# Kernel optimization log

Measured on AMD Instinct MI355X. Metric: run time of the kernel, lower is better.

Reference implementation:

```python
import jax, jax.numpy as jnp
import numpy as np

B, S, N, BS, D, H, V = 1, 2048, 128, 16, 512, 8, 32000
MASK_TOKEN_ID = 3


def setup_inputs() -> dict:
    key = jax.random.key(0)
    ks = jax.random.split(key, 10)
    anchors = jnp.sort(jax.random.randint(ks[0], (B, N), 0, S - BS), axis=1)
    return {
        "input_ids": jax.random.randint(ks[1], (B, S), 0, V),
        "hidden_states": jax.random.normal(ks[2], (B, S, D), dtype=jnp.float32),
        "loss_mask": jnp.ones((B, S), dtype=jnp.float32),
        "anchor_positions": anchors,
        "block_keep_mask": jnp.ones((B, N), dtype=bool),
        "embed_table": jax.random.normal(ks[3], (V, D), dtype=jnp.float32) * 0.02,
        "Wq": jax.random.normal(ks[4], (D, D), dtype=jnp.float32) * 0.02,
        "Wk": jax.random.normal(ks[5], (D, D), dtype=jnp.float32) * 0.02,
        "Wv": jax.random.normal(ks[6], (D, D), dtype=jnp.float32) * 0.02,
        "Wo": jax.random.normal(ks[7], (D, D), dtype=jnp.float32) * 0.02,
        "W_lm": jax.random.normal(ks[8], (D, V), dtype=jnp.float32) * 0.02,
    }


def dflash_sdpa_mask(anchor_positions, block_keep_mask):
    # KV layout: [context S | block_0 .. block_{N-1}], Q layout: [block_0 .. block_{N-1}]
    Q = N * BS
    KV = S + N * BS
    q_idx = jnp.arange(Q)              # [Q]
    kv_idx = jnp.arange(KV)            # [KV]
    q_blk = q_idx // BS                # [Q]
    anchor_q = anchor_positions[:, q_blk]          # [B,Q] anchor of each query's block
    keep_q = block_keep_mask[:, q_blk]             # [B,Q]
    is_ctx = kv_idx < S                             # [KV]
    mask_context = is_ctx[None, None, :] & (kv_idx[None, None, :] < anchor_q[:, :, None])  # [B,Q,KV]
    kv_blk = (kv_idx - S) // BS
    mask_draft = (kv_idx >= S)[None, :] & (q_blk[:, None] == kv_blk[None, :])              # [Q,KV]
    final = (mask_context | mask_draft[None]) & keep_q[:, :, None]                          # [B,Q,KV]
    return final


def reference(input_ids, hidden_states, loss_mask, anchor_positions, block_keep_mask,
              embed_table, Wq, Wk, Wv, Wo, W_lm):
    dh = D // H
    Q = N * BS

    # --- noise embedding: MASK token everywhere, anchor token at each block start ---
    safe_anchor = jnp.clip(anchor_positions, 0, S - 1)                     # [B,N]
    anchor_tokens = jnp.take_along_axis(input_ids, safe_anchor, axis=1)    # [B,N]
    start_tokens = jnp.where(block_keep_mask, anchor_tokens, MASK_TOKEN_ID)
    noise_ids = jnp.full((B, Q), MASK_TOKEN_ID, dtype=input_ids.dtype)
    noise_ids = noise_ids.at[:, jnp.arange(N) * BS].set(start_tokens)
    noise_embedding = embed_table[noise_ids]                               # [B,Q,D]

    # --- draft attention: Q = draft tokens, KV = [context hiddens | draft tokens] ---
    kv_in = jnp.concatenate([hidden_states, noise_embedding], axis=1)      # [B,S+Q,D]
    q = (noise_embedding @ Wq).reshape(B, Q, H, dh)
    k = (kv_in @ Wk).reshape(B, S + Q, H, dh)
    v = (kv_in @ Wv).reshape(B, S + Q, H, dh)
    scores = jnp.einsum("bqhd,bkhd->bhqk", q, k) / jnp.sqrt(jnp.float32(dh))
    mask = dflash_sdpa_mask(anchor_positions, block_keep_mask)[:, None]    # [B,1,Q,KV]
    attn = jax.nn.softmax(jnp.where(mask, scores, -1e9), axis=-1)
    out = jnp.einsum("bhqk,bkhd->bqhd", attn, v).reshape(B, Q, D) @ Wo     # [B,Q,D]
    logits = out @ W_lm                                                    # [B,Q,V]

    # --- block-wise CE loss ---
    offs = jnp.arange(BS)
    label_idx = anchor_positions[:, :, None] + offs[None, None, :]         # [B,N,BS]
    valid_label = label_idx < S
    safe_idx = jnp.clip(label_idx, 0, S - 1)
    ids_b = jnp.broadcast_to(input_ids[:, None, :], (B, N, S))
    target_ids = jnp.take_along_axis(ids_b, safe_idx, axis=2)              # [B,N,BS]
    lm_b = jnp.broadcast_to(loss_mask[:, None, :], (B, N, S))
    lm_g = jnp.take_along_axis(lm_b, safe_idx, axis=2)
    weight = (block_keep_mask[:, :, None].astype(jnp.float32)
              * valid_label.astype(jnp.float32)
              * (offs > 0)[None, None, :].astype(jnp.float32)
              * lm_g)                                                      # [B,N,BS]

    flat_logits = logits.reshape(-1, V)
    flat_targets = target_ids.reshape(-1)
    flat_w = weight.reshape(-1)
    logp = jax.nn.log_softmax(flat_logits, axis=-1)
    loss_per = -jnp.take_along_axis(logp, flat_targets[:, None], axis=1)[:, 0]
    loss = jnp.sum(loss_per * flat_w) / (jnp.sum(flat_w) + 1e-6)

    pred = jnp.argmax(flat_logits, axis=-1)
    correct = (pred == flat_targets) & (flat_w > 0.5)
    accuracy = jnp.sum(correct).astype(jnp.float32) / (jnp.sum(flat_w) + 1e-6)
    return loss, accuracy
```

## Files before the change

### kernel.cpp

```cpp
#include <hip/hip_runtime.h>

typedef unsigned short u16;
typedef __attribute__((ext_vector_type(4))) float f32x4;
typedef __attribute__((ext_vector_type(8))) short short8;
typedef __attribute__((ext_vector_type(4))) unsigned int uv4;
typedef __attribute__((ext_vector_type(4))) float fv4;
typedef __attribute__((ext_vector_type(4))) unsigned short usv4;

#define S_LEN 2048
#define NBLK 128
#define DMODEL 512
#define VOCAB 32000
#define QLEN 2048
#define KVLEN 4096
#define NSPLIT 250

#define GAS(p) ((const __attribute__((address_space(1))) void*)(const void*)(p))
#define LAS(p) ((__attribute__((address_space(3))) void*)(void*)(p))

__device__ __forceinline__ float bf2f(u16 u){
  union { unsigned int i; float f; } x; x.i = ((unsigned int)u) << 16; return x.f;
}
__device__ __forceinline__ u16 f2bf(float f){
  union { float f; unsigned int i; } x; x.f = f;
  unsigned int r = x.i + 0x7fffu + ((x.i >> 16) & 1u);
  return (u16)(r >> 16);
}

__global__ __launch_bounds__(256) void transpose4(const float* __restrict__ i0, const float* __restrict__ i1,
                                                  const float* __restrict__ i2, const float* __restrict__ i3,
                                                  u16* __restrict__ o0, u16* __restrict__ o1,
                                                  u16* __restrict__ o2, u16* __restrict__ o3){
  const float* in; u16* out;
  switch (blockIdx.z){
    case 0: in = i0; out = o0; break;
    case 1: in = i1; out = o1; break;
    case 2: in = i2; out = o2; break;
    default: in = i3; out = o3; break;
  }
  __shared__ float tile[32][33];
  int t = threadIdx.x, tx = t & 31, ty = t >> 5;
  int nb = blockIdx.x * 32, kb = blockIdx.y * 32;
  #pragma unroll
  for (int i = 0; i < 4; i++){
    int r = ty + i * 8;
    tile[r][tx] = in[(size_t)(kb + r) * 512 + nb + tx];
  }
  __syncthreads();
  #pragma unroll
  for (int i = 0; i < 4; i++){
    int r = ty + i * 8;
    out[(size_t)(nb + r) * 512 + kb + tx] = f2bf(tile[tx][r]);
  }
}

__global__ __launch_bounds__(256) void transpose_cast(const float* __restrict__ in,
                                                      u16* __restrict__ out,
                                                      int K, int N){
  __shared__ float tile[32][33];
  int t = threadIdx.x, tx = t & 31, ty = t >> 5;
  int nb = blockIdx.x * 32, kb = blockIdx.y * 32;
  #pragma unroll
  for (int i = 0; i < 4; i++){
    int r = ty + i * 8;
    tile[r][tx] = in[(size_t)(kb + r) * N + nb + tx];
  }
  __syncthreads();
  #pragma unroll
  for (int i = 0; i < 4; i++){
    int r = ty + i * 8;
    out[(size_t)(nb + r) * K + kb + tx] = f2bf(tile[tx][r]);
  }
}

__global__ __launch_bounds__(128) void build_kv(const float* __restrict__ hidden,
                                                const float* __restrict__ embed,
                                                const int* __restrict__ input_ids,
                                                const int* __restrict__ anchors,
                                                const unsigned char* __restrict__ keep,
                                                u16* __restrict__ kvb){
  int row = blockIdx.x;
  int t = threadIdx.x;
  const float* src;
  if (row < S_LEN){
    src = hidden + (size_t)row * DMODEL;
  } else {
    int q = row - S_LEN;
    int id = 3;
    if ((q & 15) == 0){
      int n = q >> 4;
      if (keep[n]){
        int a = anchors[n]; a = min(max(a, 0), S_LEN - 1);
        id = input_ids[a];
      }
    }
    src = embed + (size_t)id * DMODEL;
  }
  int c = t * 4;
  fv4 v = *(const fv4*)&src[c];
  usv4 o; o[0] = f2bf(v[0]); o[1] = f2bf(v[1]); o[2] = f2bf(v[2]); o[3] = f2bf(v[3]);
  *(usv4*)&kvb[(size_t)row * DMODEL + c] = o;
}

template<int TRANS, int MF>
__global__ __launch_bounds__(256) void gemmTile(const u16* __restrict__ A,
                                                const u16* __restrict__ BT,
                                                u16* __restrict__ C,
                                                int M, int N, int K, int ldc){
  __shared__ __align__(16) u16 As[2][64 * MF * 64];
  __shared__ __align__(16) u16 Bs[2][64 * 64];
  int t = threadIdx.x, w = t >> 6, lane = t & 63;
  int g = lane >> 4, li = lane & 15;
  int rowbase = blockIdx.x * (64 * MF), colbase = blockIdx.y * 64;
  int r0 = t >> 3, cg0 = t & 7;
  int swz = (cg0 ^ (r0 & 7)) << 3;

  auto stageA = [&](u16* dst, int kb){
    #pragma unroll
    for (int i = 0; i < 2 * MF; i++)
      __builtin_amdgcn_global_load_lds(GAS(&A[(size_t)(rowbase + r0 + i * 32) * K + kb + swz]),
                                       LAS(dst + i * 2048 + w * 512), 16, 0, 0);
  };
  auto stageB = [&](u16* dst, int kb){
    #pragma unroll
    for (int i = 0; i < 2; i++)
      __builtin_amdgcn_global_load_lds(GAS(&BT[(size_t)(colbase + r0 + i * 32) * K + kb + swz]),
                                       LAS(dst + i * 2048 + w * 512), 16, 0, 0);
  };

  f32x4 acc[MF][4];
  #pragma unroll
  for (int i = 0; i < MF; i++)
    #pragma unroll
    for (int j = 0; j < 4; j++)
      acc[i][j] = (f32x4){0.f, 0.f, 0.f, 0.f};

  stageA(As[0], 0); stageB(Bs[0], 0);

  int nkt = K >> 6;
  for (int kt = 0; kt < nkt; kt++){
    u16* curA = As[kt & 1]; u16* curB = Bs[kt & 1];
    if (kt + 1 < nkt){
      stageA(As[(kt + 1) & 1], (kt + 1) * 64); stageB(Bs[(kt + 1) & 1], (kt + 1) * 64);
      if constexpr (MF == 2) asm volatile("s_waitcnt vmcnt(6)" ::: "memory");
      else                   asm volatile("s_waitcnt vmcnt(4)" ::: "memory");
    } else {
      asm volatile("s_waitcnt vmcnt(0)" ::: "memory");
    }
    __builtin_amdgcn_s_barrier();
    #pragma unroll
    for (int ks = 0; ks < 2; ks++){
      short8 af[MF], bf[4];
      #pragma unroll
      for (int mf = 0; mf < MF; mf++){
        int row = w * 16 * MF + mf * 16 + li;
        af[mf] = *(const short8*)&curA[row * 64 + (((ks * 4 + g) ^ (li & 7)) << 3)];
      }
      #pragma unroll
      for (int nf = 0; nf < 4; nf++){
        int row = nf * 16 + li;
        bf[nf] = *(const short8*)&curB[row * 64 + (((ks * 4 + g) ^ (li & 7)) << 3)];
      }
      #pragma unroll
      for (int mf = 0; mf < MF; mf++)
        #pragma unroll
        for (int nf = 0; nf < 4; nf++)
          acc[mf][nf] = __builtin_amdgcn_mfma_f32_16x16x32_bf16(af[mf], bf[nf], acc[mf][nf], 0, 0, 0);
    }
    __builtin_amdgcn_s_barrier();
  }

  #pragma unroll
  for (int mf = 0; mf < MF; mf++)
    #pragma unroll
    for (int nf = 0; nf < 4; nf++)
      #pragma unroll
      for (int r = 0; r < 4; r++){
        int row = rowbase + w * 16 * MF + mf * 16 + g * 4 + r;
        int col = colbase + nf * 16 + li;
        u16 vv = f2bf(acc[mf][nf][r]);
        if (TRANS) C[(size_t)col * ldc + row] = vv;
        else       C[(size_t)row * ldc + col] = vv;
      }
}

__global__ __launch_bounds__(256) void attn_mfma(const u16* __restrict__ qb,
                                                 const u16* __restrict__ kb,
                                                 const u16* __restrict__ vT,
                                                 const int* __restrict__ anchors,
                                                 const unsigned char* __restrict__ keep,
                                                 u16* __restrict__ attnb){
  int n = blockIdx.x, h = blockIdx.y;
  int t = threadIdx.x, w = t >> 6, lane = t & 63;
  int g = lane >> 4, li = lane & 15;

  __shared__ __align__(16) u16 q_s[16][72];
  __shared__ __align__(16) u16 p_s[4][16][72];
  __shared__ float o_s[4][16][64];
  __shared__ float ml_s[4][2][16];

  {
    int r = t >> 4, c4 = (t & 15) * 4;
    *(usv4*)&q_s[r][c4] = *(const usv4*)&qb[(size_t)(n * 16 + r) * DMODEL + h * 64 + c4];
  }
  __syncthreads();

  int anchor = anchors[n];
  bool kp = keep[n] != 0;
  const u16* kh  = kb + h * 64;
  const u16* vTh = vT + (size_t)(h * 64) * KVLEN;

  if (!kp){
    if (w == 0){
      float acc = 0.f;
      const u16* row = vTh + (size_t)lane * KVLEN;
      for (int k2 = 0; k2 < KVLEN; k2 += 8){
        short8 vv = *(const short8*)&row[k2];
        #pragma unroll
        for (int j = 0; j < 8; j++) acc += bf2f((u16)vv[j]);
      }
      acc *= (1.f / 4096.f);
      u16 ov = f2bf(acc);
      for (int r = 0; r < 16; r++)
        attnb[(size_t)(n * 16 + r) * DMODEL + h * 64 + lane] = ov;
    }
    return;
  }

  short8 qa[2];
  #pragma unroll
  for (int ks = 0; ks < 2; ks++)
    qa[ks] = *(const short8*)&q_s[li][ks * 32 + g * 8];

  int nctx = (anchor + 63) >> 6;
  int ntot = nctx + 1;

  f32x4 o_acc[4];
  float m[4], l[4];
  #pragma unroll
  for (int i = 0; i < 4; i++){ o_acc[i] = (f32x4){0.f,0.f,0.f,0.f}; m[i] = -3e38f; l[i] = 0.f; }

  for (int c = w; c < ntot; c += 4){
    bool draft = (c == nctx);
    int kbase = draft ? (S_LEN + n * 16) : c * 64;
    int nk    = draft ? 16 : min(64, anchor - c * 64);

    f32x4 s[4];
    #pragma unroll
    for (int nf = 0; nf < 4; nf++) s[nf] = (f32x4){0.f,0.f,0.f,0.f};
    #pragma unroll
    for (int ks = 0; ks < 2; ks++){
      #pragma unroll
      for (int nf = 0; nf < 4; nf++){
        int krow = min(kbase + nf * 16 + li, KVLEN - 1);
        short8 bfrag = *(const short8*)&kh[(size_t)krow * DMODEL + ks * 32 + g * 8];
        s[nf] = __builtin_amdgcn_mfma_f32_16x16x32_bf16(qa[ks], bfrag, s[nf], 0, 0, 0);
      }
    }

    #pragma unroll
    for (int r = 0; r < 4; r++){
      float mx = -3e38f;
      #pragma unroll
      for (int nf = 0; nf < 4; nf++){
        float sv = s[nf][r] * 0.125f;
        if (nf * 16 + li >= nk) sv = -3e38f;
        s[nf][r] = sv;
        mx = fmaxf(mx, sv);
      }
      #pragma unroll
      for (int mm = 1; mm < 16; mm <<= 1) mx = fmaxf(mx, __shfl_xor(mx, mm));
      float mn = fmaxf(m[r], mx);
      float sc = __expf(m[r] - mn);
      float ps = 0.f;
      #pragma unroll
      for (int nf = 0; nf < 4; nf++){
        float p = __expf(s[nf][r] - mn);
        ps += p;
        p_s[w][g * 4 + r][nf * 16 + li] = f2bf(p);
      }
      #pragma unroll
      for (int mm = 1; mm < 16; mm <<= 1) ps += __shfl_xor(ps, mm);
      l[r] = l[r] * sc + ps;
      m[r] = mn;
      #pragma unroll
      for (int nfd = 0; nfd < 4; nfd++) o_acc[nfd][r] *= sc;
    }

    #pragma unroll
    for (int ks = 0; ks < 2; ks++){
      short8 pa = *(const short8*)&p_s[w][li][ks * 32 + g * 8];
      int kcol = min(kbase + ks * 32 + g * 8, KVLEN - 8);
      #pragma unroll
      for (int nfd = 0; nfd < 4; nfd++){
        short8 vfrag = *(const short8*)&vTh[(size_t)(nfd * 16 + li) * KVLEN + kcol];
        o_acc[nfd] = __builtin_amdgcn_mfma_f32_16x16x32_bf16(pa, vfrag, o_acc[nfd], 0, 0, 0);
      }
    }
  }

  #pragma unroll
  for (int r = 0; r < 4; r++){
    if (li == 0){ ml_s[w][0][g * 4 + r] = m[r]; ml_s[w][1][g * 4 + r] = l[r]; }
    #pragma unroll
    for (int nfd = 0; nfd < 4; nfd++)
      o_s[w][g * 4 + r][nfd * 16 + li] = o_acc[nfd][r];
  }
  __syncthreads();

  {
    int row = t >> 4, c0 = (t & 15) * 4;
    float M = -3e38f;
    #pragma unroll
    for (int ww = 0; ww < 4; ww++) M = fmaxf(M, ml_s[ww][0][row]);
    float L = 0.f, ew[4];
    #pragma unroll
    for (int ww = 0; ww < 4; ww++){
      ew[ww] = __expf(ml_s[ww][0][row] - M);
      L += ml_s[ww][1][row] * ew[ww];
    }
    float inv = 1.f / L;
    #pragma unroll
    for (int j = 0; j < 4; j++){
      float ov = 0.f;
      #pragma unroll
      for (int ww = 0; ww < 4; ww++) ov += o_s[ww][row][c0 + j] * ew[ww];
      attnb[(size_t)(n * 16 + row) * DMODEL + h * 64 + c0 + j] = f2bf(ov * inv);
    }
  }
}

__global__ __launch_bounds__(256) void lm_fused(const u16* __restrict__ obp,
                                                const u16* __restrict__ WT,
                                                const int* __restrict__ input_ids,
                                                const int* __restrict__ anchors,
                                                float* __restrict__ pl,
                                                float* __restrict__ pt, float* __restrict__ pbv,
                                                int* __restrict__ pbi){
  __shared__ __align__(16) u16 Wb[2][128 * 32];
  __shared__ __align__(16) u16 Ob[2][128 * 32];
  __shared__ int tcol_s[128];

  int L = blockIdx.x;
  int T = (L & 7) * 500 + (L >> 3);
  int qbase = (T & 15) * 128;
  int vb = T >> 4;
  int vocabbase = vb * 128;
  int t = threadIdx.x, w = t >> 6, lane = t & 63;
  int g = lane >> 4, li = lane & 15;
  int wv = w & 1, wq = w >> 1;

  if (t < 128){
    int r = qbase + t; int n = r >> 4, off = r & 15;
    int lab = anchors[n] + off;
    int safe = min(max(lab, 0), S_LEN - 1);
    tcol_s[t] = input_ids[safe];
  }

  int sr = t >> 2;
  int scg = (t & 3) ^ ((sr >> 1) & 3);
  auto stage = [&](u16* wdst, u16* odst, int kb){
    #pragma unroll
    for (int i = 0; i < 2; i++){
      __builtin_amdgcn_global_load_lds(GAS(&WT [(size_t)(vocabbase + i * 64 + sr) * DMODEL + kb + (scg << 3)]),
                                       LAS(wdst + i * 2048 + w * 512), 16, 0, 0);
      __builtin_amdgcn_global_load_lds(GAS(&obp[(size_t)(qbase     + i * 64 + sr) * DMODEL + kb + (scg << 3)]),
                                       LAS(odst + i * 2048 + w * 512), 16, 0, 0);
    }
  };

  f32x4 acc[4][4];
  #pragma unroll
  for (int i = 0; i < 4; i++)
    #pragma unroll
    for (int j = 0; j < 4; j++)
      acc[i][j] = (f32x4){0.f, 0.f, 0.f, 0.f};

  stage(Wb[0], Ob[0], 0);

  int cgr = (g ^ ((li >> 1) & 3)) << 3;
  for (int kt = 0; kt < 16; kt++){
    const u16* curW = Wb[kt & 1]; const u16* curO = Ob[kt & 1];
    if (kt < 15){
      stage(Wb[(kt + 1) & 1], Ob[(kt + 1) & 1], (kt + 1) * 32);
      asm volatile("s_waitcnt vmcnt(4)" ::: "memory");
    } else {
      asm volatile("s_waitcnt vmcnt(0)" ::: "memory");
    }
    __builtin_amdgcn_s_barrier();
    __builtin_amdgcn_s_setprio(1);
    short8 wfr[4], obf[4];
    #pragma unroll
    for (int vf = 0; vf < 4; vf++)
      wfr[vf] = *(const short8*)&curW[(wv * 64 + vf * 16 + li) * 32 + cgr];
    #pragma unroll
    for (int qf = 0; qf < 4; qf++)
      obf[qf] = *(const short8*)&curO[(wq * 64 + qf * 16 + li) * 32 + cgr];
    #pragma unroll
    for (int vf = 0; vf < 4; vf++)
      #pragma unroll
      for (int qf = 0; qf < 4; qf++)
        acc[vf][qf] = __builtin_amdgcn_mfma_f32_16x16x32_bf16(wfr[vf], obf[qf], acc[vf][qf], 0, 0, 0);
    __builtin_amdgcn_s_setprio(0);
    __builtin_amdgcn_s_barrier();
  }
  __syncthreads();

  u16* sb = &Wb[0][0];
  float* cse = (float*)(sb);
  float* ctv = (float*)(sb + 512);
  float* cbv = (float*)(sb + 1024);
  int*   cbi = (int*)  (sb + 1536);

  #pragma unroll
  for (int qf = 0; qf < 4; qf++){
    int qloc = wq * 64 + qf * 16 + li;
    int tc = tcol_s[qloc] - (vocabbase + wv * 64);
    float se = 0.f, tv = -3e38f, bv = -3e38f; int bi = 0x7fffffff;
    #pragma unroll
    for (int vf = 0; vf < 4; vf++){
      #pragma unroll
      for (int r = 0; r < 4; r++){
        float v = acc[vf][qf][r];
        int pos = vf * 16 + g * 4 + r;
        se += __expf(v);
        if (pos == tc) tv = v;
        if (v > bv){ bv = v; bi = pos; }
      }
    }
    #pragma unroll
    for (int off = 16; off <= 32; off <<= 1){
      se += __shfl_xor(se, off);
      tv = fmaxf(tv, __shfl_xor(tv, off));
      float ob_ = __shfl_xor(bv, off); int oi = __shfl_xor(bi, off);
      if (ob_ > bv || (ob_ == bv && oi < bi)){ bv = ob_; bi = oi; }
    }
    if (g == 0){
      cse[wv * 128 + qloc] = se; ctv[wv * 128 + qloc] = tv;
      cbv[wv * 128 + qloc] = bv; cbi[wv * 128 + qloc] = wv * 64 + bi;
    }
  }
  __syncthreads();

  if (t < 128){
    float SE = 0.f, TV = -3e38f, BV = -3e38f; int BI = 0x7fffffff;
    #pragma unroll
    for (int vv = 0; vv < 2; vv++){
      SE += cse[vv * 128 + t];
      TV = fmaxf(TV, ctv[vv * 128 + t]);
      float v = cbv[vv * 128 + t];
      if (v > BV){ BV = v; BI = cbi[vv * 128 + t]; }
    }
    size_t idx = (size_t)vb * QLEN + qbase + t;
    pl[idx] = SE; pt[idx] = TV; pbv[idx] = BV; pbi[idx] = vocabbase + BI;
  }
}

__global__ __launch_bounds__(256) void loss_rows(const float* __restrict__ pl,
                                                 const float* __restrict__ pt, const float* __restrict__ pbv,
                                                 const int* __restrict__ pbi,
                                                 const int* __restrict__ input_ids,
                                                 const int* __restrict__ anchors,
                                                 const unsigned char* __restrict__ keep,
                                                 const float* __restrict__ loss_mask,
                                                 float* __restrict__ rowacc){
  int t = threadIdx.x, w = t >> 6, lane = t & 63;
  int row = blockIdx.x * 4 + w;
  float L = 0.f, TV = -3e38f, BV = -3e38f; int BI = 0x7fffffff;
  for (int s = lane; s < NSPLIT; s += 64){
    size_t idx = (size_t)s * QLEN + row;
    L += pl[idx];
    TV = fmaxf(TV, pt[idx]);
    float bv_ = pbv[idx]; int bi_ = pbi[idx];
    if (bv_ > BV || (bv_ == BV && bi_ < BI)){ BV = bv_; BI = bi_; }
  }
  #pragma unroll
  for (int mm = 1; mm < 64; mm <<= 1){
    L += __shfl_xor(L, mm);
    TV = fmaxf(TV, __shfl_xor(TV, mm));
    float ob = __shfl_xor(BV, mm); int oi = __shfl_xor(BI, mm);
    if (ob > BV || (ob == BV && oi < BI)){ BV = ob; BI = oi; }
  }
  if (lane == 0){
    int n = row >> 4, off = row & 15;
    int lab = anchors[n] + off;
    int valid = (lab < S_LEN) ? 1 : 0;
    int safe = min(max(lab, 0), S_LEN - 1);
    int tgt = input_ids[safe];
    float wgt = (keep[n] ? 1.f : 0.f) * (valid ? 1.f : 0.f) * ((off > 0) ? 1.f : 0.f) * loss_mask[safe];
    float logp = TV - __logf(L);
    rowacc[row * 3 + 0] = -logp * wgt;
    rowacc[row * 3 + 1] = wgt;
    rowacc[row * 3 + 2] = ((BI == tgt) && (wgt > 0.5f)) ? 1.f : 0.f;
  }
}

__global__ __launch_bounds__(256) void final_sum(const float* __restrict__ rowacc, float* __restrict__ out){
  int t = threadIdx.x;
  float a = 0.f, b = 0.f, c = 0.f;
  for (int r = t; r < QLEN; r += 256){
    a += rowacc[r * 3 + 0]; b += rowacc[r * 3 + 1]; c += rowacc[r * 3 + 2];
  }
  __shared__ float sa[256], sb[256], sc_[256];
  sa[t] = a; sb[t] = b; sc_[t] = c;
  __syncthreads();
  for (int s = 128; s >= 1; s >>= 1){
    if (t < s){ sa[t] += sa[t + s]; sb[t] += sb[t + s]; sc_[t] += sc_[t + s]; }
    __syncthreads();
  }
  if (t == 0){
    out[0] = sa[0] / (sb[0] + 1e-6f);
    out[1] = sc_[0] / (sb[0] + 1e-6f);
  }
}

extern "C" void kernel_launch(void* const* d_in, const int* in_sizes, int n_in,
                              void* d_out, int out_size, void* d_ws, size_t ws_size,
                              hipStream_t stream) {
  const int*   input_ids = (const int*)  d_in[0];
  const float* hidden    = (const float*)d_in[1];
  const float* loss_mask = (const float*)d_in[2];
  const int*   anchors   = (const int*)  d_in[3];
  const unsigned char* keep = (const unsigned char*)d_in[4];
  const float* embed     = (const float*)d_in[5];
  const float* Wq        = (const float*)d_in[6];
  const float* Wk        = (const float*)d_in[7];
  const float* Wv        = (const float*)d_in[8];
  const float* Wo        = (const float*)d_in[9];
  const float* Wlm       = (const float*)d_in[10];

  char* ws = (char*)d_ws;
  size_t off = 0;
  auto take = [&](size_t bytes) -> char* {
    char* p = ws + off;
    off += (bytes + 255) & ~(size_t)255;
    return p;
  };
  u16* WqT  = (u16*)take((size_t)512 * 512 * 2);
  u16* WkT  = (u16*)take((size_t)512 * 512 * 2);
  u16* WvT  = (u16*)take((size_t)512 * 512 * 2);
  u16* WoT  = (u16*)take((size_t)512 * 512 * 2);
  u16* WlmT = (u16*)take((size_t)VOCAB * 512 * 2);
  u16* kvb  = (u16*)take((size_t)KVLEN * 512 * 2);
  u16* qb2  = (u16*)take((size_t)QLEN * 512 * 2);
  u16* kb   = (u16*)take((size_t)KVLEN * 512 * 2);
  u16* vTb  = (u16*)take((size_t)512 * KVLEN * 2);
  u16* attnb= (u16*)take((size_t)QLEN * 512 * 2);
  u16* ob   = (u16*)take((size_t)QLEN * 512 * 2);
  float* pl = (float*)take((size_t)QLEN * NSPLIT * 4);
  float* pt = (float*)take((size_t)QLEN * NSPLIT * 4);
  float* pbv= (float*)take((size_t)QLEN * NSPLIT * 4);
  int*   pbi= (int*)  take((size_t)QLEN * NSPLIT * 4);
  float* rowacc = (float*)take((size_t)QLEN * 3 * 4);

  transpose4<<<dim3(16, 16, 4), 256, 0, stream>>>(Wq, Wk, Wv, Wo, WqT, WkT, WvT, WoT);
  transpose_cast<<<dim3(1000, 16), 256, 0, stream>>>(Wlm, WlmT, 512, VOCAB);

  build_kv<<<KVLEN, 128, 0, stream>>>(hidden, embed, input_ids, anchors, keep, kvb);

  gemmTile<0, 2><<<dim3(32, 8), 256, 0, stream>>>(kvb, WkT, kb,  KVLEN, 512, 512, 512);
  gemmTile<1, 2><<<dim3(32, 8), 256, 0, stream>>>(kvb, WvT, vTb, KVLEN, 512, 512, KVLEN);
  gemmTile<0, 1><<<dim3(32, 8), 256, 0, stream>>>(kvb + (size_t)S_LEN * 512, WqT, qb2, QLEN, 512, 512, 512);

  attn_mfma<<<dim3(NBLK, 8), 256, 0, stream>>>(qb2, kb, vTb, anchors, keep, attnb);

  gemmTile<0, 1><<<dim3(32, 8), 256, 0, stream>>>(attnb, WoT, ob, QLEN, 512, 512, 512);

  lm_fused<<<4000, 256, 0, stream>>>(ob, WlmT, input_ids, anchors, pl, pt, pbv, pbi);

  loss_rows<<<512, 256, 0, stream>>>(pl, pt, pbv, pbi, input_ids, anchors, keep, loss_mask, rowacc);

  final_sum<<<1, 256, 0, stream>>>(rowacc, (float*)d_out);
}
```

Measured before the change: 235.4 us.

## Pre-swizzle LM weights into MFMA fragment layout and merge QKV GEMMs

The LM-head weight is transposed into a layout where each lane's MFMA B-fragment is one contiguous 16-byte chunk. lm_fused can then load weight fragments straight from global memory into registers, skipping LDS staging for W and halving its LDS footprint. The three Q/K/V projection GEMMs are merged into a single 640-block launch, and the Q and O projections move from 64-row to 128-row tiles. The risks are exposed global-load latency in the LM loop, now covered only by the vmcnt waits, and fewer blocks for the O projection.

```diff
diff --git a/kernel.cpp b/kernel.cpp
--- a/kernel.cpp
+++ b/kernel.cpp
@@ -54,23 +54,26 @@
   }
 }
 
-__global__ __launch_bounds__(256) void transpose_cast(const float* __restrict__ in,
-                                                      u16* __restrict__ out,
-                                                      int K, int N){
+__global__ __launch_bounds__(256) void transpose_wlm_frag(const float* __restrict__ in,
+                                                          u16* __restrict__ Wf){
   __shared__ float tile[32][33];
   int t = threadIdx.x, tx = t & 31, ty = t >> 5;
-  int nb = blockIdx.x * 32, kb = blockIdx.y * 32;
+  int vb32 = blockIdx.x, kt = blockIdx.y;
   #pragma unroll
   for (int i = 0; i < 4; i++){
     int r = ty + i * 8;
-    tile[r][tx] = in[(size_t)(kb + r) * N + nb + tx];
+    tile[r][tx] = in[(size_t)(kt * 32 + r) * VOCAB + vb32 * 32 + tx];
   }
   __syncthreads();
-  #pragma unroll
-  for (int i = 0; i < 4; i++){
-    int r = ty + i * 8;
-    out[(size_t)(nb + r) * K + kb + tx] = f2bf(tile[tx][r]);
-  }
+  int v_local = t >> 3, gg = t & 7;
+  int g = gg >> 1, j0 = (gg & 1) * 4;
+  int v = vb32 * 32 + v_local;
+  int v16 = v >> 4, li = v & 15;
+  usv4 o;
+  #pragma unroll
+  for (int jj = 0; jj < 4; jj++)
+    o[jj] = f2bf(tile[g * 8 + j0 + jj][v_local]);
+  *(usv4*)&Wf[(size_t)(((v16 * 16 + kt) * 64) + g * 16 + li) * 8 + j0] = o;
 }
 
 __global__ __launch_bounds__(128) void build_kv(const float* __restrict__ hidden,
@@ -102,58 +105,151 @@
   *(usv4*)&kvb[(size_t)row * DMODEL + c] = o;
 }
 
-template<int TRANS, int MF>
-__global__ __launch_bounds__(256) void gemmTile(const u16* __restrict__ A,
-                                                const u16* __restrict__ BT,
-                                                u16* __restrict__ C,
-                                                int M, int N, int K, int ldc){
-  __shared__ __align__(16) u16 As[2][64 * MF * 64];
+__global__ __launch_bounds__(256) void qkv_gemm(const u16* __restrict__ kvb,
+                                                const u16* __restrict__ WkT,
+                                                const u16* __restrict__ WvT,
+                                                const u16* __restrict__ WqT,
+                                                u16* __restrict__ kb,
+                                                u16* __restrict__ vTb,
+                                                u16* __restrict__ qb2){
+  __shared__ __align__(16) u16 As[2][128 * 64];
+  __shared__ __align__(16) u16 Bs[2][64 * 64];
+  int id = blockIdx.x;
+  const u16* A = kvb; const u16* BT; u16* C; int ldc; int trans = 0;
+  int rowbase, colbase;
+  if (id < 256){
+    BT = WkT; C = kb; ldc = 512;
+    rowbase = (id & 31) * 128; colbase = (id >> 5) * 64;
+  } else if (id < 512){
+    int j = id - 256;
+    BT = WvT; C = vTb; ldc = KVLEN; trans = 1;
+    rowbase = (j & 31) * 128; colbase = (j >> 5) * 64;
+  } else {
+    int j = id - 512;
+    A = kvb + (size_t)S_LEN * DMODEL;
+    BT = WqT; C = qb2; ldc = 512;
+    rowbase = (j & 15) * 128; colbase = (j >> 4) * 64;
+  }
+  int t = threadIdx.x, w = t >> 6, lane = t & 63;
+  int g = lane >> 4, li = lane & 15;
+  int r0 = t >> 3, cg0 = t & 7;
+  int swz = (cg0 ^ (r0 & 7)) << 3;
+
+  auto stageA = [&](u16* dst, int kb_){
+    #pragma unroll
+    for (int i = 0; i < 4; i++)
+      __builtin_amdgcn_global_load_lds(GAS(&A[(size_t)(rowbase + r0 + i * 32) * DMODEL + kb_ + swz]),
+                                       LAS(dst + i * 2048 + w * 512), 16, 0, 0);
+  };
+  auto stageB = [&](u16* dst, int kb_){
+    #pragma unroll
+    for (int i = 0; i < 2; i++)
+      __builtin_amdgcn_global_load_lds(GAS(&BT[(size_t)(colbase + r0 + i * 32) * DMODEL + kb_ + swz]),
+                                       LAS(dst + i * 2048 + w * 512), 16, 0, 0);
+  };
+
+  f32x4 acc[2][4];
+  #pragma unroll
+  for (int i = 0; i < 2; i++)
+    #pragma unroll
+    for (int j = 0; j < 4; j++)
+      acc[i][j] = (f32x4){0.f, 0.f, 0.f, 0.f};
+
+  stageA(As[0], 0); stageB(Bs[0], 0);
+
+  for (int kt = 0; kt < 8; kt++){
+    u16* curA = As[kt & 1]; u16* curB = Bs[kt & 1];
+    if (kt < 7){
+      stageA(As[(kt + 1) & 1], (kt + 1) * 64); stageB(Bs[(kt + 1) & 1], (kt + 1) * 64);
+      asm volatile("s_waitcnt vmcnt(6)" ::: "memory");
+    } else {
+      asm volatile("s_waitcnt vmcnt(0)" ::: "memory");
+    }
+    __builtin_amdgcn_s_barrier();
+    #pragma unroll
+    for (int ks = 0; ks < 2; ks++){
+      short8 af[2], bf[4];
+      #pragma unroll
+      for (int mf = 0; mf < 2; mf++){
+        int row = w * 32 + mf * 16 + li;
+        af[mf] = *(const short8*)&curA[row * 64 + (((ks * 4 + g) ^ (li & 7)) << 3)];
+      }
+      #pragma unroll
+      for (int nf = 0; nf < 4; nf++){
+        int row = nf * 16 + li;
+        bf[nf] = *(const short8*)&curB[row * 64 + (((ks * 4 + g) ^ (li & 7)) << 3)];
+      }
+      #pragma unroll
+      for (int mf = 0; mf < 2; mf++)
+        #pragma unroll
+        for (int nf = 0; nf < 4; nf++)
+          acc[mf][nf] = __builtin_amdgcn_mfma_f32_16x16x32_bf16(af[mf], bf[nf], acc[mf][nf], 0, 0, 0);
+    }
+    __builtin_amdgcn_s_barrier();
+  }
+
+  #pragma unroll
+  for (int mf = 0; mf < 2; mf++)
+    #pragma unroll
+    for (int nf = 0; nf < 4; nf++)
+      #pragma unroll
+      for (int r = 0; r < 4; r++){
+        int row = rowbase + w * 32 + mf * 16 + g * 4 + r;
+        int col = colbase + nf * 16 + li;
+        u16 vv = f2bf(acc[mf][nf][r]);
+        if (trans) C[(size_t)col * ldc + row] = vv;
+        else       C[(size_t)row * ldc + col] = vv;
+      }
+}
+
+__global__ __launch_bounds__(256) void gemmO(const u16* __restrict__ A,
+                                             const u16* __restrict__ BT,
+                                             u16* __restrict__ C){
+  __shared__ __align__(16) u16 As[2][128 * 64];
   __shared__ __align__(16) u16 Bs[2][64 * 64];
   int t = threadIdx.x, w = t >> 6, lane = t & 63;
   int g = lane >> 4, li = lane & 15;
-  int rowbase = blockIdx.x * (64 * MF), colbase = blockIdx.y * 64;
+  int rowbase = blockIdx.x * 128, colbase = blockIdx.y * 64;
   int r0 = t >> 3, cg0 = t & 7;
   int swz = (cg0 ^ (r0 & 7)) << 3;
 
-  auto stageA = [&](u16* dst, int kb){
-    #pragma unroll
-    for (int i = 0; i < 2 * MF; i++)
-      __builtin_amdgcn_global_load_lds(GAS(&A[(size_t)(rowbase + r0 + i * 32) * K + kb + swz]),
+  auto stageA = [&](u16* dst, int kb_){
+    #pragma unroll
+    for (int i = 0; i < 4; i++)
+      __builtin_amdgcn_global_load_lds(GAS(&A[(size_t)(rowbase + r0 + i * 32) * DMODEL + kb_ + swz]),
                                        LAS(dst + i * 2048 + w * 512), 16, 0, 0);
   };
-  auto stageB = [&](u16* dst, int kb){
+  auto stageB = [&](u16* dst, int kb_){
     #pragma unroll
     for (int i = 0; i < 2; i++)
-      __builtin_amdgcn_global_load_lds(GAS(&BT[(size_t)(colbase + r0 + i * 32) * K + kb + swz]),
+      __builtin_amdgcn_global_load_lds(GAS(&BT[(size_t)(colbase + r0 + i * 32) * DMODEL + kb_ + swz]),
                                        LAS(dst + i * 2048 + w * 512), 16, 0, 0);
   };
 
-  f32x4 acc[MF][4];
-  #pragma unroll
-  for (int i = 0; i < MF; i++)
+  f32x4 acc[2][4];
+  #pragma unroll
+  for (int i = 0; i < 2; i++)
     #pragma unroll
     for (int j = 0; j < 4; j++)
       acc[i][j] = (f32x4){0.f, 0.f, 0.f, 0.f};
 
   stageA(As[0], 0); stageB(Bs[0], 0);
 
-  int nkt = K >> 6;
-  for (int kt = 0; kt < nkt; kt++){
+  for (int kt = 0; kt < 8; kt++){
     u16* curA = As[kt & 1]; u16* curB = Bs[kt & 1];
-    if (kt + 1 < nkt){
+    if (kt < 7){
       stageA(As[(kt + 1) & 1], (kt + 1) * 64); stageB(Bs[(kt + 1) & 1], (kt + 1) * 64);
-      if constexpr (MF == 2) asm volatile("s_waitcnt vmcnt(6)" ::: "memory");
-      else                   asm volatile("s_waitcnt vmcnt(4)" ::: "memory");
+      asm volatile("s_waitcnt vmcnt(6)" ::: "memory");
     } else {
       asm volatile("s_waitcnt vmcnt(0)" ::: "memory");
     }
     __builtin_amdgcn_s_barrier();
     #pragma unroll
     for (int ks = 0; ks < 2; ks++){
-      short8 af[MF], bf[4];
-      #pragma unroll
-      for (int mf = 0; mf < MF; mf++){
-        int row = w * 16 * MF + mf * 16 + li;
+      short8 af[2], bf[4];
+      #pragma unroll
+      for (int mf = 0; mf < 2; mf++){
+        int row = w * 32 + mf * 16 + li;
         af[mf] = *(const short8*)&curA[row * 64 + (((ks * 4 + g) ^ (li & 7)) << 3)];
       }
       #pragma unroll
@@ -162,7 +258,7 @@
         bf[nf] = *(const short8*)&curB[row * 64 + (((ks * 4 + g) ^ (li & 7)) << 3)];
       }
       #pragma unroll
-      for (int mf = 0; mf < MF; mf++)
+      for (int mf = 0; mf < 2; mf++)
         #pragma unroll
         for (int nf = 0; nf < 4; nf++)
           acc[mf][nf] = __builtin_amdgcn_mfma_f32_16x16x32_bf16(af[mf], bf[nf], acc[mf][nf], 0, 0, 0);
@@ -171,16 +267,14 @@
   }
 
   #pragma unroll
-  for (int mf = 0; mf < MF; mf++)
+  for (int mf = 0; mf < 2; mf++)
     #pragma unroll
     for (int nf = 0; nf < 4; nf++)
       #pragma unroll
       for (int r = 0; r < 4; r++){
-        int row = rowbase + w * 16 * MF + mf * 16 + g * 4 + r;
+        int row = rowbase + w * 32 + mf * 16 + g * 4 + r;
         int col = colbase + nf * 16 + li;
-        u16 vv = f2bf(acc[mf][nf][r]);
-        if (TRANS) C[(size_t)col * ldc + row] = vv;
-        else       C[(size_t)row * ldc + col] = vv;
+        C[(size_t)row * DMODEL + col] = f2bf(acc[mf][nf][r]);
       }
 }
 
@@ -331,13 +425,12 @@
 }
 
 __global__ __launch_bounds__(256) void lm_fused(const u16* __restrict__ obp,
-                                                const u16* __restrict__ WT,
+                                                const u16* __restrict__ Wf,
                                                 const int* __restrict__ input_ids,
                                                 const int* __restrict__ anchors,
                                                 float* __restrict__ pl,
                                                 float* __restrict__ pt, float* __restrict__ pbv,
                                                 int* __restrict__ pbi){
-  __shared__ __align__(16) u16 Wb[2][128 * 32];
   __shared__ __align__(16) u16 Ob[2][128 * 32];
   __shared__ int tcol_s[128];
 
@@ -359,15 +452,13 @@
 
   int sr = t >> 2;
   int scg = (t & 3) ^ ((sr >> 1) & 3);
-  auto stage = [&](u16* wdst, u16* odst, int kb){
-    #pragma unroll
-    for (int i = 0; i < 2; i++){
-      __builtin_amdgcn_global_load_lds(GAS(&WT [(size_t)(vocabbase + i * 64 + sr) * DMODEL + kb + (scg << 3)]),
-                                       LAS(wdst + i * 2048 + w * 512), 16, 0, 0);
-      __builtin_amdgcn_global_load_lds(GAS(&obp[(size_t)(qbase     + i * 64 + sr) * DMODEL + kb + (scg << 3)]),
+  auto stageO = [&](u16* odst, int kt){
+    #pragma unroll
+    for (int i = 0; i < 2; i++)
+      __builtin_amdgcn_global_load_lds(GAS(&obp[(size_t)(qbase + i * 64 + sr) * DMODEL + kt * 32 + (scg << 3)]),
                                        LAS(odst + i * 2048 + w * 512), 16, 0, 0);
-    }
   };
+  const u16* wbase = Wf + ((size_t)(vb * 8 + wv * 4) * 16) * 512 + lane * 8;
 
   f32x4 acc[4][4];
   #pragma unroll
@@ -376,23 +467,27 @@
     for (int j = 0; j < 4; j++)
       acc[i][j] = (f32x4){0.f, 0.f, 0.f, 0.f};
 
-  stage(Wb[0], Ob[0], 0);
+  stageO(Ob[0], 0);
 
   int cgr = (g ^ ((li >> 1) & 3)) << 3;
   for (int kt = 0; kt < 16; kt++){
-    const u16* curW = Wb[kt & 1]; const u16* curO = Ob[kt & 1];
+    const u16* curO = Ob[kt & 1];
+    short8 wfr[4];
     if (kt < 15){
-      stage(Wb[(kt + 1) & 1], Ob[(kt + 1) & 1], (kt + 1) * 32);
+      stageO(Ob[(kt + 1) & 1], kt + 1);
+      #pragma unroll
+      for (int vf = 0; vf < 4; vf++)
+        wfr[vf] = *(const short8*)(wbase + ((size_t)(vf * 16 + kt) * 64) * 8);
+      asm volatile("s_waitcnt vmcnt(6)" ::: "memory");
+    } else {
+      #pragma unroll
+      for (int vf = 0; vf < 4; vf++)
+        wfr[vf] = *(const short8*)(wbase + ((size_t)(vf * 16 + kt) * 64) * 8);
       asm volatile("s_waitcnt vmcnt(4)" ::: "memory");
-    } else {
-      asm volatile("s_waitcnt vmcnt(0)" ::: "memory");
     }
     __builtin_amdgcn_s_barrier();
     __builtin_amdgcn_s_setprio(1);
-    short8 wfr[4], obf[4];
-    #pragma unroll
-    for (int vf = 0; vf < 4; vf++)
-      wfr[vf] = *(const short8*)&curW[(wv * 64 + vf * 16 + li) * 32 + cgr];
+    short8 obf[4];
     #pragma unroll
     for (int qf = 0; qf < 4; qf++)
       obf[qf] = *(const short8*)&curO[(wq * 64 + qf * 16 + li) * 32 + cgr];
@@ -406,11 +501,10 @@
   }
   __syncthreads();
 
-  u16* sb = &Wb[0][0];
-  float* cse = (float*)(sb);
-  float* ctv = (float*)(sb + 512);
-  float* cbv = (float*)(sb + 1024);
-  int*   cbi = (int*)  (sb + 1536);
+  float* cse = (float*)&Ob[0][0];
+  float* ctv = (float*)&Ob[0][512];
+  float* cbv = (float*)&Ob[0][1024];
+  int*   cbi = (int*)  &Ob[0][1536];
 
   #pragma unroll
   for (int qf = 0; qf < 4; qf++){
@@ -540,7 +634,7 @@
   u16* WkT  = (u16*)take((size_t)512 * 512 * 2);
   u16* WvT  = (u16*)take((size_t)512 * 512 * 2);
   u16* WoT  = (u16*)take((size_t)512 * 512 * 2);
-  u16* WlmT = (u16*)take((size_t)VOCAB * 512 * 2);
+  u16* Wfrag= (u16*)take((size_t)VOCAB * 512 * 2);
   u16* kvb  = (u16*)take((size_t)KVLEN * 512 * 2);
   u16* qb2  = (u16*)take((size_t)QLEN * 512 * 2);
   u16* kb   = (u16*)take((size_t)KVLEN * 512 * 2);
@@ -554,19 +648,17 @@
   float* rowacc = (float*)take((size_t)QLEN * 3 * 4);
 
   transpose4<<<dim3(16, 16, 4), 256, 0, stream>>>(Wq, Wk, Wv, Wo, WqT, WkT, WvT, WoT);
-  transpose_cast<<<dim3(1000, 16), 256, 0, stream>>>(Wlm, WlmT, 512, VOCAB);
+  transpose_wlm_frag<<<dim3(1000, 16), 256, 0, stream>>>(Wlm, Wfrag);
 
   build_kv<<<KVLEN, 128, 0, stream>>>(hidden, embed, input_ids, anchors, keep, kvb);
 
-  gemmTile<0, 2><<<dim3(32, 8), 256, 0, stream>>>(kvb, WkT, kb,  KVLEN, 512, 512, 512);
-  gemmTile<1, 2><<<dim3(32, 8), 256, 0, stream>>>(kvb, WvT, vTb, KVLEN, 512, 512, KVLEN);
-  gemmTile<0, 1><<<dim3(32, 8), 256, 0, stream>>>(kvb + (size_t)S_LEN * 512, WqT, qb2, QLEN, 512, 512, 512);
+  qkv_gemm<<<640, 256, 0, stream>>>(kvb, WkT, WvT, WqT, kb, vTb, qb2);
 
   attn_mfma<<<dim3(NBLK, 8), 256, 0, stream>>>(qb2, kb, vTb, anchors, keep, attnb);
 
-  gemmTile<0, 1><<<dim3(32, 8), 256, 0, stream>>>(attnb, WoT, ob, QLEN, 512, 512, 512);
-
-  lm_fused<<<4000, 256, 0, stream>>>(ob, WlmT, input_ids, anchors, pl, pt, pbv, pbi);
+  gemmO<<<dim3(16, 8), 256, 0, stream>>>(attnb, WoT, ob);
+
+  lm_fused<<<4000, 256, 0, stream>>>(ob, Wfrag, input_ids, anchors, pl, pt, pbv, pbi);
 
   loss_rows<<<512, 256, 0, stream>>>(pl, pt, pbv, pbi, input_ids, anchors, keep, loss_mask, rowacc);
 
```

New measurement: 222.9 us. 1.06x faster.
